# Optimization experiments

Hardware: AMD Instinct MI355X
Metric: run time of the kernel (lower is better)

## Reference

```python
import jax, jax.numpy as jnp
import numpy as np
import math

HIDDEN = 512
BATCH, SEQ = 4, 4096


def setup_inputs() -> dict:
    key = jax.random.key(0)
    ks = jax.random.split(key, 7)
    s = 1.0 / math.sqrt(HIDDEN)
    return {
        "X": jax.random.normal(ks[0], (BATCH, SEQ, HIDDEN), dtype=jnp.float32),
        "Wq": jax.random.uniform(ks[1], (HIDDEN, HIDDEN), jnp.float32, -s, s),
        "bq": jax.random.uniform(ks[2], (HIDDEN,), jnp.float32, -s, s),
        "Wk": jax.random.uniform(ks[3], (HIDDEN, HIDDEN), jnp.float32, -s, s),
        "bk": jax.random.uniform(ks[4], (HIDDEN,), jnp.float32, -s, s),
        "Wv": jax.random.uniform(ks[5], (HIDDEN, HIDDEN), jnp.float32, -s, s),
        "bv": jax.random.uniform(ks[6], (HIDDEN,), jnp.float32, -s, s),
    }


def reference(X, Wq, bq, Wk, bk, Wv, bv):
    # Q, K, V projections (torch Linear: y = x @ W.T + b; here W stored as [in, out])
    Q = jnp.einsum("bsd,de->bse", X, Wq) + bq
    K = jnp.einsum("bsd,de->bse", X, Wk) + bk
    V = jnp.einsum("bsd,de->bse", X, Wv) + bv
    scale = 1.0 / math.sqrt(Q.shape[-1])
    scores = jnp.einsum("bqd,bkd->bqk", Q, K) * scale  # [B, S, S]
    weights = jax.nn.softmax(scores, axis=-1)
    return jnp.einsum("bqk,bkd->bqd", weights, V)
```

## Files before the change

### kernel.cpp

```cpp
#include <hip/hip_runtime.h>
#include <hip/hip_bf16.h>
#include <math.h>


typedef __bf16 bfx8 __attribute__((ext_vector_type(8)));
typedef __bf16 bfx4 __attribute__((ext_vector_type(4)));
typedef float  fx4  __attribute__((ext_vector_type(4)));

#define HID   512
#define NBATCH 4
#define SEQ   4096
#define MROWS (NBATCH * SEQ)

#if __has_builtin(__builtin_amdgcn_exp2f)
#define EXPFN(x) __builtin_amdgcn_exp2f(x)
#define QSCALE 0.06375871589f
#else
#define EXPFN(x) __expf(x)
#define QSCALE 0.04419417382f
#endif

constexpr int MODE_QKV = 0;
constexpr int MODE_EXP = 2;
constexpr int MODE_DIV = 3;

__device__ __forceinline__ void gload_lds16(const __bf16* gsrc, __bf16* ldst) {
  __builtin_amdgcn_global_load_lds(
      (const __attribute__((address_space(1))) unsigned int*)gsrc,
      (__attribute__((address_space(3))) unsigned int*)ldst,
      16, 0, 0);
}

__global__ void prep_x_kernel(const float* __restrict__ X, __bf16* __restrict__ Xb) {
  int i = (blockIdx.x * 256 + threadIdx.x) * 4;
  const float4 v = *(const float4*)(X + i);
  bfx4 o;
  o[0] = (__bf16)v.x; o[1] = (__bf16)v.y; o[2] = (__bf16)v.z; o[3] = (__bf16)v.w;
  *(bfx4*)(Xb + i) = o;
}

__global__ void prep_w_kernel(const float* __restrict__ Wq, const float* __restrict__ Wk,
                              const float* __restrict__ Wv, __bf16* __restrict__ Wt) {
  int id  = blockIdx.x * 256 + threadIdx.x;
  int g   = id >> 18;
  int rem = id & ((1 << 18) - 1);
  int i   = rem >> 9;
  int o   = rem & 511;
  const float* W = (g == 0) ? Wq : ((g == 1) ? Wk : Wv);
  Wt[(g << 18) + (o << 9) + i] = (__bf16)W[rem];
}

template <int MODE, int TM, int TN>
__global__ __launch_bounds__(256)
void gemm_bt(const __bf16* __restrict__ A, const __bf16* __restrict__ B,
             void* __restrict__ C0v, void* __restrict__ C1v, void* __restrict__ C2v,
             const float* __restrict__ b0, const float* __restrict__ b1,
             const float* __restrict__ b2, float* __restrict__ rowsum,
             int lda, int ldb, int ldc, int K_,
             long sA, long sB, long sC, int sR) {
  constexpr int MT = TM / 32;
  constexpr int NT = TN / 32;
  constexpr int ABE = (TM + TN) * 64;
  constexpr int CTE = (MODE == MODE_DIV) ? TM * TN * 2 : TM * TN;
  constexpr int LDSN = (ABE > CTE) ? ABE : CTE;
  __shared__ __bf16 L[LDSN];
  __bf16* As = L;
  __bf16* Bs = L + TM * 64;

  const int z = blockIdx.z;
  A += (long)z * sA;
  B += (long)z * sB;

  const int tid  = threadIdx.x;
  const int lane = tid & 63;
  const int w    = tid >> 6;
  const int wm   = w >> 1, wn = w & 1;
  const int lm   = lane & 15, lq = lane >> 4;

  const int row0 = blockIdx.y * TM;
  const int col0 = blockIdx.x * TN;

  const __bf16* Ag = A + (long)row0 * lda;
  const __bf16* Bg = B + (long)col0 * ldb;

  fx4 acc[MT][NT] = {};

  for (int kt = 0; kt < K_; kt += 64) {
    __syncthreads();
#pragma unroll
    for (int it = 0; it < TM / 32; ++it) {
      int s = it * 256 + tid;
      int r = s >> 3, c = ((s & 7) ^ (r & 7)) << 3;
      gload_lds16(Ag + (long)r * lda + kt + c, As + it * 2048 + w * 512);
    }
#pragma unroll
    for (int it = 0; it < TN / 32; ++it) {
      int s = it * 256 + tid;
      int r = s >> 3, c = ((s & 7) ^ (r & 7)) << 3;
      gload_lds16(Bg + (long)r * ldb + kt + c, Bs + it * 2048 + w * 512);
    }
    __syncthreads();
#pragma unroll
    for (int kk = 0; kk < 2; ++kk) {
      bfx8 af[MT], bfr[NT];
#pragma unroll
      for (int t = 0; t < MT; ++t) {
        int ra = wm * (TM / 2) + t * 16 + lm;
        af[t] = *(const bfx8*)(As + ra * 64 + (((kk * 4 + lq) ^ (ra & 7)) << 3));
      }
#pragma unroll
      for (int t = 0; t < NT; ++t) {
        int rb = wn * (TN / 2) + t * 16 + lm;
        bfr[t] = *(const bfx8*)(Bs + rb * 64 + (((kk * 4 + lq) ^ (rb & 7)) << 3));
      }
#pragma unroll
      for (int mt = 0; mt < MT; ++mt)
#pragma unroll
        for (int nt = 0; nt < NT; ++nt)
          acc[mt][nt] = __builtin_amdgcn_mfma_f32_16x16x32_bf16(af[mt], bfr[nt],
                                                                acc[mt][nt], 0, 0, 0);
    }
  }

  const int lr0 = wm * (TM / 2);
  const int lc0 = wn * (TN / 2);

  __syncthreads();

  if constexpr (MODE == MODE_QKV) {
    const int g   = col0 >> 9;
    const int gc  = col0 & 511;
    const float* bias = (g == 0) ? b0 : ((g == 1) ? b1 : b2);
    float bvv[NT];
#pragma unroll
    for (int nt = 0; nt < NT; ++nt) bvv[nt] = bias[gc + lc0 + nt * 16 + lm];

    if (g < 2) {
      __bf16* Ct = L;
#pragma unroll
      for (int mt = 0; mt < MT; ++mt)
#pragma unroll
        for (int nt = 0; nt < NT; ++nt)
#pragma unroll
          for (int i = 0; i < 4; ++i) {
            float v = acc[mt][nt][i] + bvv[nt];
            if (g == 0) v *= QSCALE;
            Ct[(lr0 + mt * 16 + lq * 4 + i) * TN + lc0 + nt * 16 + lm] = (__bf16)v;
          }
      __syncthreads();
      __bf16* C = (g == 0) ? (__bf16*)C0v : (__bf16*)C1v;
#pragma unroll
      for (int j = 0; j < TM * TN / 2048; ++j) {
        int s = j * 256 + tid;
        int off = s * 8;
        int r = off / TN, c = off % TN;
        *(bfx8*)(C + (long)(row0 + r) * ldc + gc + c) = *(const bfx8*)(Ct + off);
      }
    } else {
      __bf16* C = (__bf16*)C2v;
#pragma unroll
      for (int mt = 0; mt < MT; ++mt)
#pragma unroll
        for (int nt = 0; nt < NT; ++nt) {
          int c  = gc + lc0 + nt * 16 + lm;
          int rb = row0 + lr0 + mt * 16 + lq * 4;
          int b  = rb >> 12;
          int s  = rb & 4095;
          bfx4 pk;
#pragma unroll
          for (int i = 0; i < 4; ++i) pk[i] = (__bf16)(acc[mt][nt][i] + bvv[nt]);
          *(bfx4*)(C + ((long)b * HID + c) * SEQ + s) = pk;
        }
    }
  } else if constexpr (MODE == MODE_EXP) {
    __bf16* Ct = L;
    float* rsump = rowsum + (long)z * sR;
#pragma unroll
    for (int mt = 0; mt < MT; ++mt)
#pragma unroll
      for (int i = 0; i < 4; ++i) {
        int rl = lr0 + mt * 16 + lq * 4 + i;
        float rs = 0.f;
#pragma unroll
        for (int nt = 0; nt < NT; ++nt) {
          float e = EXPFN(acc[mt][nt][i]);
          Ct[rl * TN + lc0 + nt * 16 + lm] = (__bf16)e;
          rs += e;
        }
        rs += __shfl_xor(rs, 1);
        rs += __shfl_xor(rs, 2);
        rs += __shfl_xor(rs, 4);
        rs += __shfl_xor(rs, 8);
        if (lm == 0) atomicAdd(&rsump[row0 + rl], rs);
      }
    __syncthreads();
    __bf16* C = ((__bf16*)C0v) + (long)z * sC;
#pragma unroll
    for (int j = 0; j < TM * TN / 2048; ++j) {
      int s = j * 256 + tid;
      int off = s * 8;
      int r = off / TN, c = off % TN;
      *(bfx8*)(C + (long)(row0 + r) * ldc + col0 + c) = *(const bfx8*)(Ct + off);
    }
  } else {
    float* Cf = (float*)L;
    const float* rsump = rowsum + (long)z * sR;
#pragma unroll
    for (int mt = 0; mt < MT; ++mt)
#pragma unroll
      for (int i = 0; i < 4; ++i) {
        int rl = lr0 + mt * 16 + lq * 4 + i;
        float inv = 1.f / rsump[row0 + rl];
#pragma unroll
        for (int nt = 0; nt < NT; ++nt)
          Cf[rl * TN + lc0 + nt * 16 + lm] = acc[mt][nt][i] * inv;
      }
    __syncthreads();
    float* C = ((float*)C0v) + (long)z * sC;
#pragma unroll
    for (int j = 0; j < TM * TN / 1024; ++j) {
      int s = j * 256 + tid;
      int off = s * 4;
      int r = off / TN, c = off % TN;
      *(float4*)(C + (long)(row0 + r) * ldc + col0 + c) = *(const float4*)(Cf + off);
    }
  }
}

extern "C" void kernel_launch(void* const* d_in, const int* in_sizes, int n_in,
                              void* d_out, int out_size, void* d_ws, size_t ws_size,
                              hipStream_t stream) {
  (void)in_sizes; (void)n_in; (void)out_size; (void)ws_size;
  const float* X  = (const float*)d_in[0];
  const float* Wq = (const float*)d_in[1];
  const float* bq = (const float*)d_in[2];
  const float* Wk = (const float*)d_in[3];
  const float* bk = (const float*)d_in[4];
  const float* Wv = (const float*)d_in[5];
  const float* bv = (const float*)d_in[6];
  float* out = (float*)d_out;

  __bf16* Xb     = (__bf16*)d_ws;
  __bf16* Wt     = Xb + (long)MROWS * HID;
  __bf16* Q      = Wt + 3 * HID * HID;
  __bf16* Kb     = Q + (long)MROWS * HID;
  __bf16* Vt     = Kb + (long)MROWS * HID;
  float*  rowsum = (float*)(Vt + (long)MROWS * HID);
  __bf16* E      = (__bf16*)(rowsum + MROWS);

  prep_x_kernel<<<(MROWS * HID) / 1024, 256, 0, stream>>>(X, Xb);
  prep_w_kernel<<<(3 * HID * HID) / 256, 256, 0, stream>>>(Wq, Wk, Wv, Wt);

  (void)hipMemsetAsync(rowsum, 0, MROWS * sizeof(float), stream);

  gemm_bt<MODE_QKV, 128, 128><<<dim3(12, 128, 1), 256, 0, stream>>>(
      Xb, Wt, Q, Kb, Vt, bq, bk, bv, nullptr,
      HID, HID, HID, HID, 0, 0, 0, 0);

  gemm_bt<MODE_EXP, 128, 128><<<dim3(32, 32, NBATCH), 256, 0, stream>>>(
      Q, Kb, E, nullptr, nullptr, nullptr, nullptr, nullptr, rowsum,
      HID, HID, SEQ, HID, (long)SEQ * HID, (long)SEQ * HID, (long)SEQ * SEQ, SEQ);

  gemm_bt<MODE_DIV, 64, 128><<<dim3(4, 64, NBATCH), 256, 0, stream>>>(
      E, Vt, out, nullptr, nullptr, nullptr, nullptr, nullptr, rowsum,
      SEQ, SEQ, HID, SEQ, (long)SEQ * SEQ, (long)HID * SEQ, (long)SEQ * HID, SEQ);
}
```

Before: 327.2 us.

## Double-buffer GEMM LDS tiles with async prefetch and padded epilogue staging

Turns the GEMM main loop into a two-stage software pipeline. The next K tile is fetched with global_load_lds into an alternate LDS buffer while MFMAs run on the current one, and synchronisation uses explicit vmcnt waits and raw barriers. K-step depth becomes a template parameter: 32 for the QKV and QK^T GEMMs, 64 for PV, with the XOR swizzle adjusted to match. The epilogue staging buffer gets a padded row pitch to cut LDS bank conflicts. The cost is more LDS per block (possible occupancy loss) and a second barrier per iteration.

```diff
diff --git a/kernel.cpp b/kernel.cpp
--- a/kernel.cpp
+++ b/kernel.cpp
@@ -23,6 +23,8 @@
 constexpr int MODE_QKV = 0;
 constexpr int MODE_EXP = 2;
 constexpr int MODE_DIV = 3;
+
+constexpr int WVM(int n) { return (n & 15) | ((n >> 4) << 14) | (7 << 4) | (15 << 8); }
 
 __device__ __forceinline__ void gload_lds16(const __bf16* gsrc, __bf16* ldst) {
   __builtin_amdgcn_global_load_lds(
@@ -50,7 +52,7 @@
   Wt[(g << 18) + (o << 9) + i] = (__bf16)W[rem];
 }
 
-template <int MODE, int TM, int TN>
+template <int MODE, int TM, int TN, int BK>
 __global__ __launch_bounds__(256)
 void gemm_bt(const __bf16* __restrict__ A, const __bf16* __restrict__ B,
              void* __restrict__ C0v, void* __restrict__ C1v, void* __restrict__ C2v,
@@ -58,14 +60,20 @@
              const float* __restrict__ b2, float* __restrict__ rowsum,
              int lda, int ldb, int ldc, int K_,
              long sA, long sB, long sC, int sR) {
-  constexpr int MT = TM / 32;
-  constexpr int NT = TN / 32;
-  constexpr int ABE = (TM + TN) * 64;
-  constexpr int CTE = (MODE == MODE_DIV) ? TM * TN * 2 : TM * TN;
-  constexpr int LDSN = (ABE > CTE) ? ABE : CTE;
+  constexpr int MT  = TM / 32;
+  constexpr int NT  = TN / 32;
+  constexpr int CH  = BK / 8;
+  constexpr int LCH = (CH == 8) ? 3 : 2;
+  constexpr int SH  = (CH == 8) ? 0 : 1;
+  constexpr int NKK = BK / 32;
+  constexpr int SBE = (TM + TN) * BK;
+  constexpr int CP  = TN + 8;
+  constexpr int CTE = (MODE == MODE_DIV) ? TM * CP * 2 : TM * CP;
+  constexpr int LDSN = (2 * SBE > CTE) ? 2 * SBE : CTE;
+  constexpr int LPT_A = TM * CH / 256;
+  constexpr int LPT_B = TN * CH / 256;
+  constexpr int LPT   = LPT_A + LPT_B;
   __shared__ __bf16 L[LDSN];
-  __bf16* As = L;
-  __bf16* Bs = L + TM * 64;
 
   const int z = blockIdx.z;
   A += (long)z * sA;
@@ -83,35 +91,52 @@
   const __bf16* Ag = A + (long)row0 * lda;
   const __bf16* Bg = B + (long)col0 * ldb;
 
+  auto issue_tile = [&](int ktv, int p) {
+    __bf16* Ad = L + p * SBE;
+    __bf16* Bd = Ad + TM * BK;
+#pragma unroll
+    for (int j = 0; j < LPT_A; ++j) {
+      int s = j * 256 + tid;
+      int r = s >> LCH, cp = s & (CH - 1);
+      int cl = cp ^ ((r >> SH) & (CH - 1));
+      gload_lds16(Ag + (long)r * lda + ktv + cl * 8, Ad + j * 2048 + w * 512);
+    }
+#pragma unroll
+    for (int j = 0; j < LPT_B; ++j) {
+      int s = j * 256 + tid;
+      int r = s >> LCH, cp = s & (CH - 1);
+      int cl = cp ^ ((r >> SH) & (CH - 1));
+      gload_lds16(Bg + (long)r * ldb + ktv + cl * 8, Bd + j * 2048 + w * 512);
+    }
+  };
+
   fx4 acc[MT][NT] = {};
-
-  for (int kt = 0; kt < K_; kt += 64) {
-    __syncthreads();
-#pragma unroll
-    for (int it = 0; it < TM / 32; ++it) {
-      int s = it * 256 + tid;
-      int r = s >> 3, c = ((s & 7) ^ (r & 7)) << 3;
-      gload_lds16(Ag + (long)r * lda + kt + c, As + it * 2048 + w * 512);
-    }
-#pragma unroll
-    for (int it = 0; it < TN / 32; ++it) {
-      int s = it * 256 + tid;
-      int r = s >> 3, c = ((s & 7) ^ (r & 7)) << 3;
-      gload_lds16(Bg + (long)r * ldb + kt + c, Bs + it * 2048 + w * 512);
-    }
-    __syncthreads();
-#pragma unroll
-    for (int kk = 0; kk < 2; ++kk) {
+  const int NI = K_ / BK;
+
+  issue_tile(0, 0);
+  for (int iter = 0; iter < NI; ++iter) {
+    if (iter + 1 < NI) {
+      issue_tile((iter + 1) * BK, (iter + 1) & 1);
+      __builtin_amdgcn_s_waitcnt(WVM(LPT));
+    } else {
+      __builtin_amdgcn_s_waitcnt(WVM(0));
+    }
+    __builtin_amdgcn_s_barrier();
+    __builtin_amdgcn_sched_barrier(0);
+    const __bf16* Asp = L + (iter & 1) * SBE;
+    const __bf16* Bsp = Asp + TM * BK;
+#pragma unroll
+    for (int kk = 0; kk < NKK; ++kk) {
       bfx8 af[MT], bfr[NT];
 #pragma unroll
       for (int t = 0; t < MT; ++t) {
         int ra = wm * (TM / 2) + t * 16 + lm;
-        af[t] = *(const bfx8*)(As + ra * 64 + (((kk * 4 + lq) ^ (ra & 7)) << 3));
+        af[t] = *(const bfx8*)(Asp + ra * BK + (((kk * 4 + lq) ^ ((ra >> SH) & (CH - 1))) << 3));
       }
 #pragma unroll
       for (int t = 0; t < NT; ++t) {
         int rb = wn * (TN / 2) + t * 16 + lm;
-        bfr[t] = *(const bfx8*)(Bs + rb * 64 + (((kk * 4 + lq) ^ (rb & 7)) << 3));
+        bfr[t] = *(const bfx8*)(Bsp + rb * BK + (((kk * 4 + lq) ^ ((rb >> SH) & (CH - 1))) << 3));
       }
 #pragma unroll
       for (int mt = 0; mt < MT; ++mt)
@@ -120,6 +145,8 @@
           acc[mt][nt] = __builtin_amdgcn_mfma_f32_16x16x32_bf16(af[mt], bfr[nt],
                                                                 acc[mt][nt], 0, 0, 0);
     }
+    __builtin_amdgcn_sched_barrier(0);
+    __builtin_amdgcn_s_barrier();
   }
 
   const int lr0 = wm * (TM / 2);
@@ -145,7 +172,7 @@
           for (int i = 0; i < 4; ++i) {
             float v = acc[mt][nt][i] + bvv[nt];
             if (g == 0) v *= QSCALE;
-            Ct[(lr0 + mt * 16 + lq * 4 + i) * TN + lc0 + nt * 16 + lm] = (__bf16)v;
+            Ct[(lr0 + mt * 16 + lq * 4 + i) * CP + lc0 + nt * 16 + lm] = (__bf16)v;
           }
       __syncthreads();
       __bf16* C = (g == 0) ? (__bf16*)C0v : (__bf16*)C1v;
@@ -154,7 +181,7 @@
         int s = j * 256 + tid;
         int off = s * 8;
         int r = off / TN, c = off % TN;
-        *(bfx8*)(C + (long)(row0 + r) * ldc + gc + c) = *(const bfx8*)(Ct + off);
+        *(bfx8*)(C + (long)(row0 + r) * ldc + gc + c) = *(const bfx8*)(Ct + r * CP + c);
       }
     } else {
       __bf16* C = (__bf16*)C2v;
@@ -184,7 +211,7 @@
 #pragma unroll
         for (int nt = 0; nt < NT; ++nt) {
           float e = EXPFN(acc[mt][nt][i]);
-          Ct[rl * TN + lc0 + nt * 16 + lm] = (__bf16)e;
+          Ct[rl * CP + lc0 + nt * 16 + lm] = (__bf16)e;
           rs += e;
         }
         rs += __shfl_xor(rs, 1);
@@ -200,7 +227,7 @@
       int s = j * 256 + tid;
       int off = s * 8;
       int r = off / TN, c = off % TN;
-      *(bfx8*)(C + (long)(row0 + r) * ldc + col0 + c) = *(const bfx8*)(Ct + off);
+      *(bfx8*)(C + (long)(row0 + r) * ldc + col0 + c) = *(const bfx8*)(Ct + r * CP + c);
     }
   } else {
     float* Cf = (float*)L;
@@ -213,7 +240,7 @@
         float inv = 1.f / rsump[row0 + rl];
 #pragma unroll
         for (int nt = 0; nt < NT; ++nt)
-          Cf[rl * TN + lc0 + nt * 16 + lm] = acc[mt][nt][i] * inv;
+          Cf[rl * CP + lc0 + nt * 16 + lm] = acc[mt][nt][i] * inv;
       }
     __syncthreads();
     float* C = ((float*)C0v) + (long)z * sC;
@@ -222,7 +249,7 @@
       int s = j * 256 + tid;
       int off = s * 4;
       int r = off / TN, c = off % TN;
-      *(float4*)(C + (long)(row0 + r) * ldc + col0 + c) = *(const float4*)(Cf + off);
+      *(float4*)(C + (long)(row0 + r) * ldc + col0 + c) = *(const float4*)(Cf + r * CP + c);
     }
   }
 }
@@ -253,15 +280,15 @@
 
   (void)hipMemsetAsync(rowsum, 0, MROWS * sizeof(float), stream);
 
-  gemm_bt<MODE_QKV, 128, 128><<<dim3(12, 128, 1), 256, 0, stream>>>(
+  gemm_bt<MODE_QKV, 128, 128, 32><<<dim3(12, 128, 1), 256, 0, stream>>>(
       Xb, Wt, Q, Kb, Vt, bq, bk, bv, nullptr,
       HID, HID, HID, HID, 0, 0, 0, 0);
 
-  gemm_bt<MODE_EXP, 128, 128><<<dim3(32, 32, NBATCH), 256, 0, stream>>>(
+  gemm_bt<MODE_EXP, 128, 128, 32><<<dim3(32, 32, NBATCH), 256, 0, stream>>>(
       Q, Kb, E, nullptr, nullptr, nullptr, nullptr, nullptr, rowsum,
       HID, HID, SEQ, HID, (long)SEQ * HID, (long)SEQ * HID, (long)SEQ * SEQ, SEQ);
 
-  gemm_bt<MODE_DIV, 64, 128><<<dim3(4, 64, NBATCH), 256, 0, stream>>>(
+  gemm_bt<MODE_DIV, 64, 128, 64><<<dim3(4, 64, NBATCH), 256, 0, stream>>>(
       E, Vt, out, nullptr, nullptr, nullptr, nullptr, nullptr, rowsum,
       SEQ, SEQ, HID, SEQ, (long)SEQ * SEQ, (long)HID * SEQ, (long)SEQ * HID, SEQ);
 }
```

Measured after the change: 332.7 us. No clear change (+1.7%).
